# Performance work log

Hardware: AMD Instinct MI355X
Metric: run time of the kernel (lower is better)

The kernel has to match this reference:

```python
import jax, jax.numpy as jnp
import numpy as np

N = 100000      # nodes
E = 1600000     # directed edges (avg degree 16)
F_IN = 256      # dataset.num_node_features
HID = 64        # hidden
C = 40          # dataset.num_classes


def setup_inputs() -> dict:
    key = jax.random.key(0)
    k0, k1, k2, k3 = jax.random.split(key, 4)
    x = jax.random.normal(k0, (N, F_IN), dtype=jnp.float32)
    edge_index = jax.random.randint(k1, (2, E), 0, N, dtype=jnp.int32)
    # Glorot-style init like GCNConv.reset_parameters
    W1 = jax.random.normal(k2, (F_IN, HID), dtype=jnp.float32) * (1.0 / np.sqrt(F_IN))
    b1 = jnp.zeros((HID,), dtype=jnp.float32)
    W2 = jax.random.normal(k3, (HID, C), dtype=jnp.float32) * (1.0 / np.sqrt(HID))
    b2 = jnp.zeros((C,), dtype=jnp.float32)
    return {"x": x, "edge_index": edge_index, "W1": W1, "b1": b1, "W2": W2, "b2": b2}


def gcn_conv(x, row, col, norm, W, b):
    # PyG GCNConv: out[col] += norm * (x @ W)[row]; then + bias
    n = x.shape[0]
    h = x @ W                                   # [N, out]
    msg = h[row] * norm[:, None]                # [E+N, out] gather + scale
    out = jax.ops.segment_sum(msg, col, num_segments=n)  # scatter-add
    return out + b


def _norm_coeffs(edge_index, n, dtype):
    # add self-loops, then symmetric normalization D^{-1/2} A D^{-1/2}
    loop = jnp.arange(n, dtype=edge_index.dtype)
    row = jnp.concatenate([edge_index[0], loop])
    col = jnp.concatenate([edge_index[1], loop])
    deg = jax.ops.segment_sum(jnp.ones_like(col, dtype=dtype), col, num_segments=n)
    dis = jnp.where(deg > 0, jax.lax.rsqrt(jnp.maximum(deg, 1.0)), 0.0)
    return row, col, dis[row] * dis[col]


def reference(x, edge_index, W1, b1, W2, b2):
    n = x.shape[0]
    row, col, norm = _norm_coeffs(edge_index, n, x.dtype)
    h = jax.nn.relu(gcn_conv(x, row, col, norm, W1, b1))
    # F.dropout(p=0.5, training=False) is identity in eval mode
    out = gcn_conv(h, row, col, norm, W2, b2)
    return jax.nn.log_softmax(out, axis=1)
```

## Files before the change

kernel.cpp:

```cpp
#include <hip/hip_runtime.h>
#include <math.h>

#define N_NODES 100000
#define N_EDGES 1600000
#define F_INDIM 256
#define HID 64
#define NCLS 40
#define NBKT 196
#define BKT_CAP 10240
#define EPB 8192
#define ESRC_CAP 1904640

typedef __attribute__((ext_vector_type(8))) short short8;
typedef __attribute__((ext_vector_type(4))) float floatx4;

__device__ __forceinline__ unsigned short f2bf(float f) {
  unsigned u = __float_as_uint(f);
  unsigned r = (u + 0x7FFFu + ((u >> 16) & 1u)) >> 16;
  return (unsigned short)r;
}
__device__ __forceinline__ void add8(float* a, uint4 u) {
  a[0] += __uint_as_float(u.x << 16);
  a[1] += __uint_as_float(u.x & 0xFFFF0000u);
  a[2] += __uint_as_float(u.y << 16);
  a[3] += __uint_as_float(u.y & 0xFFFF0000u);
  a[4] += __uint_as_float(u.z << 16);
  a[5] += __uint_as_float(u.z & 0xFFFF0000u);
  a[6] += __uint_as_float(u.w << 16);
  a[7] += __uint_as_float(u.w & 0xFFFF0000u);
}


__global__ __launch_bounds__(256) void k_zero(int* __restrict__ gcur,
                                              unsigned int* __restrict__ h1bw) {
  int t = threadIdx.x;
  if (t < NBKT) gcur[t] = 0;
  if (t < 32) h1bw[(size_t)N_NODES * 32 + t] = 0;
}


__global__ __launch_bounds__(1024) void k_binA(const int* __restrict__ row,
                                               const int* __restrict__ col,
                                               int* __restrict__ gcur,
                                               unsigned int* __restrict__ bktdata) {
  __shared__ int hist[NBKT];
  __shared__ int cur[NBKT];
  __shared__ int gbase[NBKT];
  const int t = threadIdx.x;
  const int e0 = blockIdx.x * EPB;
  const int n = min(EPB, N_EDGES - e0);
  if (t < NBKT) hist[t] = 0;
  __syncthreads();
  for (int i = t * 4; i < n; i += 4096) {
    int4 c4 = *(const int4*)&col[e0 + i];
    atomicAdd(&hist[c4.x >> 9], 1);
    atomicAdd(&hist[c4.y >> 9], 1);
    atomicAdd(&hist[c4.z >> 9], 1);
    atomicAdd(&hist[c4.w >> 9], 1);
  }
  __syncthreads();
  if (t < NBKT) {
    cur[t] = 0;
    int h = hist[t];
    gbase[t] = (h > 0) ? atomicAdd(&gcur[t], h) : 0;
  }
  __syncthreads();
  for (int i = t * 4; i < n; i += 4096) {
    int4 c4 = *(const int4*)&col[e0 + i];
    int4 r4 = *(const int4*)&row[e0 + i];
#pragma unroll
    for (int k = 0; k < 4; ++k) {
      int c = (k == 0) ? c4.x : (k == 1) ? c4.y : (k == 2) ? c4.z : c4.w;
      int r = (k == 0) ? r4.x : (k == 1) ? r4.y : (k == 2) ? r4.z : r4.w;
      int b = c >> 9;
      int p = atomicAdd(&cur[b], 1);
      bktdata[(size_t)b * BKT_CAP + gbase[b] + p] =
          ((unsigned)(c & 511) << 17) | (unsigned)r;
    }
  }
}


__global__ __launch_bounds__(1024) void k_build2(const int* __restrict__ gcur,
                                                 const unsigned int* __restrict__ bktdata,
                                                 float* __restrict__ dis,
                                                 int* __restrict__ start,
                                                 int* __restrict__ endi,
                                                 int* __restrict__ esrc) {
  __shared__ int h[512];
  __shared__ int cur[512];
  __shared__ int sbase[512];
  __shared__ int wsum[4];
  const int b = blockIdx.x, t = threadIdx.x;
  if (t < 512) { h[t] = 0; cur[t] = 0; }
  if (t < 256) {
    int pv = (t < b) ? (((gcur[t] + 3) & ~3) + 1536) : 0;
#pragma unroll
    for (int off = 1; off < 64; off <<= 1) pv += __shfl_xor(pv, off);
    if ((t & 63) == 0) wsum[t >> 6] = pv;
  }
  __syncthreads();
  const int base = wsum[0] + wsum[1] + wsum[2] + wsum[3];

  const int cnt = gcur[b];
  const unsigned int* p = bktdata + (size_t)b * BKT_CAP;
  for (int i = t; i < cnt; i += 1024) atomicAdd(&h[p[i] >> 17], 1);
  __syncthreads();

  int c0 = 0, p0 = 0;
  if (t < 512) {
    const int n0 = b * 512 + t;
    c0 = h[t];
    p0 = (c0 + 3) & ~3;
    if (n0 < N_NODES) dis[n0] = rsqrtf((float)(c0 + 1));
    h[t] = p0;
  }
  __syncthreads();
#pragma unroll
  for (int off = 1; off < 512; off <<= 1) {
    int u = (t < 512 && t >= off) ? h[t - off] : 0;
    __syncthreads();
    if (t < 512) h[t] += u;
    __syncthreads();
  }
  if (t < 512) {
    const int n0 = b * 512 + t;
    const int sb0 = base + h[t] - p0;
    sbase[t] = sb0;
    if (n0 < N_NODES) { start[n0] = sb0; endi[n0] = sb0 + c0; }
    for (int k = c0; k < p0; ++k) esrc[sb0 + k] = N_NODES;
    if (b == 0 && t == 0) start[N_NODES] = N_EDGES;
  }
  __syncthreads();

  for (int i = t; i < cnt; i += 1024) {
    unsigned u = p[i];
    int ld = u >> 17;
    int src = u & 0x1FFFF;
    int pos = sbase[ld] + atomicAdd(&cur[ld], 1);
    esrc[pos] = src;
  }
}


#define KP 264

__global__ __launch_bounds__(256) void k_gemm1(const float* __restrict__ x,
                                               const float* __restrict__ W1,
                                               const float* __restrict__ dis,
                                               unsigned short* __restrict__ h1b) {
  __shared__ unsigned short wt[HID * KP];
  const int tid = threadIdx.x;
  const int lane = tid & 63;
  const int w = tid >> 6;
  const int quad = lane >> 4;
  const int l15 = lane & 15;
  const int rowBase = blockIdx.x * 64;

#pragma unroll
  for (int i = 0; i < 16; ++i) {
    int f = tid + 256 * i;
    int k = f >> 4;
    int n0 = (f & 15) * 4;
    float4 v = *(const float4*)&W1[(size_t)k * HID + n0];
    wt[(n0 + 0) * KP + k] = f2bf(v.x);
    wt[(n0 + 1) * KP + k] = f2bf(v.y);
    wt[(n0 + 2) * KP + k] = f2bf(v.z);
    wt[(n0 + 3) * KP + k] = f2bf(v.w);
  }
  __syncthreads();

  const int ar = rowBase + w * 16 + l15;
  const float* xrow = x + (size_t)((ar < N_NODES) ? ar : N_NODES - 1) * F_INDIM + quad * 8;

  floatx4 acc[4];
#pragma unroll
  for (int c = 0; c < 4; ++c) acc[c] = (floatx4){0.f, 0.f, 0.f, 0.f};

#pragma unroll
  for (int kc = 0; kc < F_INDIM; kc += 32) {
    const float4 va = *(const float4*)(xrow + kc);
    const float4 vb = *(const float4*)(xrow + kc + 4);
    short8 a;
    a[0] = (short)f2bf(va.x); a[1] = (short)f2bf(va.y);
    a[2] = (short)f2bf(va.z); a[3] = (short)f2bf(va.w);
    a[4] = (short)f2bf(vb.x); a[5] = (short)f2bf(vb.y);
    a[6] = (short)f2bf(vb.z); a[7] = (short)f2bf(vb.w);
#pragma unroll
    for (int c = 0; c < 4; ++c) {
      const short8 b = *(const short8*)&wt[(c * 16 + l15) * KP + kc + quad * 8];
      acc[c] = __builtin_amdgcn_mfma_f32_16x16x32_bf16(a, b, acc[c], 0, 0, 0);
    }
  }

#pragma unroll
  for (int reg = 0; reg < 4; ++reg) {
    int gr = rowBase + w * 16 + quad * 4 + reg;
    if (gr < N_NODES) {
      float d = dis[gr];
#pragma unroll
      for (int c = 0; c < 4; ++c)
        h1b[(size_t)gr * HID + c * 16 + l15] = f2bf(d * acc[c][reg]);
    }
  }
}


__global__ __launch_bounds__(256) void k_agg1(const int* __restrict__ esrc,
                                              const int* __restrict__ start,
                                              const int* __restrict__ endi,
                                              const float* __restrict__ dis,
                                              const unsigned short* __restrict__ h1b,
                                              const float* __restrict__ b1,
                                              unsigned short* __restrict__ ab) {
  int gid = blockIdx.x * 256 + threadIdx.x;
  int node = gid >> 3;
  int q = gid & 7;
  if (node >= N_NODES) return;
  const uint4* hp4 = (const uint4*)h1b;
  const int s = start[node];
  const int epad = (endi[node] + 3) & ~3;
  float acc[8];
#pragma unroll
  for (int j = 0; j < 8; ++j) acc[j] = 0.f;
  int i = s;
  for (; i + 8 <= epad; i += 8) {
    int4 sa = *(const int4*)&esrc[i];
    int4 sb = *(const int4*)&esrc[i + 4];
    uint4 u0 = hp4[(size_t)sa.x * 8 + q];
    uint4 u1 = hp4[(size_t)sa.y * 8 + q];
    uint4 u2 = hp4[(size_t)sa.z * 8 + q];
    uint4 u3 = hp4[(size_t)sa.w * 8 + q];
    uint4 u4 = hp4[(size_t)sb.x * 8 + q];
    uint4 u5 = hp4[(size_t)sb.y * 8 + q];
    uint4 u6 = hp4[(size_t)sb.z * 8 + q];
    uint4 u7 = hp4[(size_t)sb.w * 8 + q];
    add8(acc, u0); add8(acc, u1); add8(acc, u2); add8(acc, u3);
    add8(acc, u4); add8(acc, u5); add8(acc, u6); add8(acc, u7);
  }
  if (i < epad) {
    int4 sv = *(const int4*)&esrc[i];
    uint4 u0 = hp4[(size_t)sv.x * 8 + q];
    uint4 u1 = hp4[(size_t)sv.y * 8 + q];
    uint4 u2 = hp4[(size_t)sv.z * 8 + q];
    uint4 u3 = hp4[(size_t)sv.w * 8 + q];
    add8(acc, u0); add8(acc, u1); add8(acc, u2); add8(acc, u3);
  }
  uint4 us = hp4[(size_t)node * 8 + q];
  add8(acc, us);
  float d = dis[node];
  float4 ba = *(const float4*)&b1[q * 8];
  float4 bb = *(const float4*)&b1[q * 8 + 4];
  float v0 = fmaxf(d * acc[0] + ba.x, 0.f);
  float v1 = fmaxf(d * acc[1] + ba.y, 0.f);
  float v2 = fmaxf(d * acc[2] + ba.z, 0.f);
  float v3 = fmaxf(d * acc[3] + ba.w, 0.f);
  float v4 = fmaxf(d * acc[4] + bb.x, 0.f);
  float v5 = fmaxf(d * acc[5] + bb.y, 0.f);
  float v6 = fmaxf(d * acc[6] + bb.z, 0.f);
  float v7 = fmaxf(d * acc[7] + bb.w, 0.f);
  uint4 o;
  o.x = (unsigned)f2bf(v0) | ((unsigned)f2bf(v1) << 16);
  o.y = (unsigned)f2bf(v2) | ((unsigned)f2bf(v3) << 16);
  o.z = (unsigned)f2bf(v4) | ((unsigned)f2bf(v5) << 16);
  o.w = (unsigned)f2bf(v6) | ((unsigned)f2bf(v7) << 16);
  ((uint4*)ab)[(size_t)node * 8 + q] = o;
}


#define AP 72

__global__ __launch_bounds__(256) void k_gemm2(const unsigned short* __restrict__ ab,
                                               const float* __restrict__ W2,
                                               const float* __restrict__ dis,
                                               unsigned short* __restrict__ gb) {
  __shared__ unsigned short as[64 * AP];
  __shared__ unsigned short w2t[48 * AP];
  const int tid = threadIdx.x;
  const int lane = tid & 63;
  const int w = tid >> 6;
  const int quad = lane >> 4;
  const int l15 = lane & 15;
  const int rowBase = blockIdx.x * 64;

  for (int i = tid; i < 48 * 64; i += 256) {
    int n = i >> 6;
    int k = i & 63;
    w2t[n * AP + k] = (n < NCLS) ? f2bf(W2[(size_t)k * NCLS + n]) : (unsigned short)0;
  }
#pragma unroll
  for (int i = 0; i < 2; ++i) {
    int f = tid + 256 * i;
    int r = f >> 3;
    int q = f & 7;
    int gr = rowBase + r;
    short8 v = (short8){0, 0, 0, 0, 0, 0, 0, 0};
    if (gr < N_NODES) v = *(const short8*)&ab[(size_t)gr * HID + q * 8];
    *(short8*)&as[r * AP + q * 8] = v;
  }
  __syncthreads();

  floatx4 acc[3];
#pragma unroll
  for (int c = 0; c < 3; ++c) acc[c] = (floatx4){0.f, 0.f, 0.f, 0.f};

#pragma unroll
  for (int kh = 0; kh < 2; ++kh) {
    const short8 a = *(const short8*)&as[(w * 16 + l15) * AP + kh * 32 + quad * 8];
#pragma unroll
    for (int c = 0; c < 3; ++c) {
      const short8 b = *(const short8*)&w2t[(c * 16 + l15) * AP + kh * 32 + quad * 8];
      acc[c] = __builtin_amdgcn_mfma_f32_16x16x32_bf16(a, b, acc[c], 0, 0, 0);
    }
  }

#pragma unroll
  for (int reg = 0; reg < 4; ++reg) {
    int gr = rowBase + w * 16 + quad * 4 + reg;
    if (gr < N_NODES) {
      float d = dis[gr];
#pragma unroll
      for (int c = 0; c < 3; ++c) {
        int cc = c * 16 + l15;
        gb[(size_t)gr * 64 + cc] = f2bf(d * acc[c][reg]);
      }
      gb[(size_t)gr * 64 + 48 + l15] = 0;
    }
  }
}


__global__ __launch_bounds__(256) void k_agg2ls(const int* __restrict__ esrc,
                                                const int* __restrict__ start,
                                                const int* __restrict__ endi,
                                                const float* __restrict__ dis,
                                                const unsigned short* __restrict__ gb,
                                                const float* __restrict__ b2,
                                                float* __restrict__ out) {
  int gid = blockIdx.x * 256 + threadIdx.x;
  int node = gid >> 3;
  int q = gid & 7;
  if (node >= N_NODES) return;
  const uint4* gp4 = (const uint4*)gb;
  const int s = start[node];
  const int epad = (endi[node] + 3) & ~3;
  float acc[8];
#pragma unroll
  for (int j = 0; j < 8; ++j) acc[j] = 0.f;
  int i = s;
  for (; i + 8 <= epad; i += 8) {
    int4 sa = *(const int4*)&esrc[i];
    int4 sb = *(const int4*)&esrc[i + 4];
    uint4 u0 = gp4[(size_t)sa.x * 8 + q];
    uint4 u1 = gp4[(size_t)sa.y * 8 + q];
    uint4 u2 = gp4[(size_t)sa.z * 8 + q];
    uint4 u3 = gp4[(size_t)sa.w * 8 + q];
    uint4 u4 = gp4[(size_t)sb.x * 8 + q];
    uint4 u5 = gp4[(size_t)sb.y * 8 + q];
    uint4 u6 = gp4[(size_t)sb.z * 8 + q];
    uint4 u7 = gp4[(size_t)sb.w * 8 + q];
    add8(acc, u0); add8(acc, u1); add8(acc, u2); add8(acc, u3);
    add8(acc, u4); add8(acc, u5); add8(acc, u6); add8(acc, u7);
  }
  if (i < epad) {
    int4 sv = *(const int4*)&esrc[i];
    uint4 u0 = gp4[(size_t)sv.x * 8 + q];
    uint4 u1 = gp4[(size_t)sv.y * 8 + q];
    uint4 u2 = gp4[(size_t)sv.z * 8 + q];
    uint4 u3 = gp4[(size_t)sv.w * 8 + q];
    add8(acc, u0); add8(acc, u1); add8(acc, u2); add8(acc, u3);
  }
  uint4 us = gp4[(size_t)node * 8 + q];
  add8(acc, us);
  const bool wr = q < 5;
  float v0 = 0.f, v1 = 0.f, v2 = 0.f, v3 = 0.f, v4 = 0.f, v5 = 0.f, v6 = 0.f, v7 = 0.f;
  float m = -INFINITY;
  if (wr) {
    float d = dis[node];
    float4 ba = *(const float4*)&b2[q * 8];
    float4 bb = *(const float4*)&b2[q * 8 + 4];
    v0 = d * acc[0] + ba.x;
    v1 = d * acc[1] + ba.y;
    v2 = d * acc[2] + ba.z;
    v3 = d * acc[3] + ba.w;
    v4 = d * acc[4] + bb.x;
    v5 = d * acc[5] + bb.y;
    v6 = d * acc[6] + bb.z;
    v7 = d * acc[7] + bb.w;
    m = fmaxf(fmaxf(fmaxf(v0, v1), fmaxf(v2, v3)),
              fmaxf(fmaxf(v4, v5), fmaxf(v6, v7)));
  }
#pragma unroll
  for (int off = 1; off < 8; off <<= 1) m = fmaxf(m, __shfl_xor(m, off));
  float el = 0.f;
  if (wr) {
    el = __expf(v0 - m) + __expf(v1 - m) + __expf(v2 - m) + __expf(v3 - m) +
         __expf(v4 - m) + __expf(v5 - m) + __expf(v6 - m) + __expf(v7 - m);
  }
#pragma unroll
  for (int off = 1; off < 8; off <<= 1) el += __shfl_xor(el, off);
  float ls = logf(el);
  if (wr) {
    float4 o1 = make_float4(v0 - m - ls, v1 - m - ls, v2 - m - ls, v3 - m - ls);
    float4 o2 = make_float4(v4 - m - ls, v5 - m - ls, v6 - m - ls, v7 - m - ls);
    *(float4*)&out[(size_t)node * NCLS + q * 8] = o1;
    *(float4*)&out[(size_t)node * NCLS + q * 8 + 4] = o2;
  }
}


extern "C" void kernel_launch(void* const* d_in, const int* in_sizes, int n_in,
                              void* d_out, int out_size, void* d_ws, size_t ws_size,
                              hipStream_t stream) {
  const float* x  = (const float*)d_in[0];
  const int*   ei = (const int*)d_in[1];
  const float* W1 = (const float*)d_in[2];
  const float* b1 = (const float*)d_in[3];
  const float* W2 = (const float*)d_in[4];
  const float* b2 = (const float*)d_in[5];
  float* out = (float*)d_out;

  const int* row = ei;
  const int* col = ei + N_EDGES;

  int*            esrc    = (int*)d_ws;
  unsigned int*   bktdata = (unsigned int*)(esrc + ESRC_CAP);
  unsigned short* h1b     = (unsigned short*)(bktdata + (size_t)NBKT * BKT_CAP);
  unsigned short* ab      = h1b + (size_t)(N_NODES + 1) * HID;
  float*          dis     = (float*)(ab + (size_t)N_NODES * HID);
  int*            start   = (int*)(dis + N_NODES);
  int*            endi    = start + N_NODES + 1;
  int*            gcur    = endi + N_NODES;
  unsigned short* gb      = h1b;

  k_zero<<<1, 256, 0, stream>>>(gcur, (unsigned int*)h1b);
  k_binA<<<(N_EDGES + EPB - 1) / EPB, 1024, 0, stream>>>(row, col, gcur, bktdata);
  k_build2<<<NBKT, 1024, 0, stream>>>(gcur, bktdata, dis, start, endi, esrc);

  k_gemm1<<<(N_NODES + 63) / 64, 256, 0, stream>>>(x, W1, dis, h1b);
  k_agg1<<<(N_NODES * 8 + 255) / 256, 256, 0, stream>>>(esrc, start, endi, dis, h1b, b1, ab);

  k_gemm2<<<(N_NODES + 63) / 64, 256, 0, stream>>>(ab, W2, dis, gb);
  k_agg2ls<<<(N_NODES * 8 + 255) / 256, 256, 0, stream>>>(esrc, start, endi, dis, gb, b2, out);
}
```

Baseline: 288.9 us.

## Fuse edge binning with GEMM1 and aggregation1 with GEMM2, drop global atomics

Edge binning and the first GEMM now run as one kernel whose blocks take different roles, so GEMM1 no longer waits on the degree computation. Source-side normalization moves into the aggregation, which reads dis per neighbor. Binning writes fixed-capacity per-block slots instead of using a global atomic cursor, which removes the zeroing kernel. Layer-1 aggregation and GEMM2 are fused through shared memory, cutting launches and the intermediate round trip. The cost is extra per-edge dis loads and fixed capacities (CAPB=96, ECAP) that assume the uniform random degree distribution and can silently drop edges if a per-block bucket overflows.

Result: slower. 316.2 us (+9.5%).

```diff
diff --git a/kernel.cpp b/kernel.cpp
--- a/kernel.cpp
+++ b/kernel.cpp
@@ -7,9 +7,14 @@
 #define HID 64
 #define NCLS 40
 #define NBKT 196
-#define BKT_CAP 10240
+#define NBLKA 196
 #define EPB 8192
-#define ESRC_CAP 1904640
+#define CAPB 96
+#define REGSZ 12544
+#define ECAP 10240
+#define NGEMM1 391
+#define KP 264
+#define AP 72
 
 typedef __attribute__((ext_vector_type(8))) short short8;
 typedef __attribute__((ext_vector_type(4))) float floatx4;
@@ -29,90 +34,158 @@
   a[6] += __uint_as_float(u.w << 16);
   a[7] += __uint_as_float(u.w & 0xFFFF0000u);
 }
-
-
-__global__ __launch_bounds__(256) void k_zero(int* __restrict__ gcur,
-                                              unsigned int* __restrict__ h1bw) {
-  int t = threadIdx.x;
-  if (t < NBKT) gcur[t] = 0;
-  if (t < 32) h1bw[(size_t)N_NODES * 32 + t] = 0;
-}
-
-
-__global__ __launch_bounds__(1024) void k_binA(const int* __restrict__ row,
-                                               const int* __restrict__ col,
-                                               int* __restrict__ gcur,
-                                               unsigned int* __restrict__ bktdata) {
-  __shared__ int hist[NBKT];
-  __shared__ int cur[NBKT];
-  __shared__ int gbase[NBKT];
+__device__ __forceinline__ void fma8(float* a, float d, uint4 u) {
+  a[0] = fmaf(d, __uint_as_float(u.x << 16), a[0]);
+  a[1] = fmaf(d, __uint_as_float(u.x & 0xFFFF0000u), a[1]);
+  a[2] = fmaf(d, __uint_as_float(u.y << 16), a[2]);
+  a[3] = fmaf(d, __uint_as_float(u.y & 0xFFFF0000u), a[3]);
+  a[4] = fmaf(d, __uint_as_float(u.z << 16), a[4]);
+  a[5] = fmaf(d, __uint_as_float(u.z & 0xFFFF0000u), a[5]);
+  a[6] = fmaf(d, __uint_as_float(u.w << 16), a[6]);
+  a[7] = fmaf(d, __uint_as_float(u.w & 0xFFFF0000u), a[7]);
+}
+
+
+__global__ __launch_bounds__(1024) void k_pre(const int* __restrict__ row,
+                                              const int* __restrict__ col,
+                                              const float* __restrict__ x,
+                                              const float* __restrict__ W1,
+                                              unsigned int* __restrict__ bktdata,
+                                              int* __restrict__ cnt,
+                                              unsigned short* __restrict__ h1b) {
+  __shared__ union {
+    int cur[NBKT];
+    unsigned short wt[HID * KP];
+  } sm;
   const int t = threadIdx.x;
-  const int e0 = blockIdx.x * EPB;
-  const int n = min(EPB, N_EDGES - e0);
-  if (t < NBKT) hist[t] = 0;
-  __syncthreads();
-  for (int i = t * 4; i < n; i += 4096) {
-    int4 c4 = *(const int4*)&col[e0 + i];
-    atomicAdd(&hist[c4.x >> 9], 1);
-    atomicAdd(&hist[c4.y >> 9], 1);
-    atomicAdd(&hist[c4.z >> 9], 1);
-    atomicAdd(&hist[c4.w >> 9], 1);
-  }
-  __syncthreads();
-  if (t < NBKT) {
-    cur[t] = 0;
-    int h = hist[t];
-    gbase[t] = (h > 0) ? atomicAdd(&gcur[t], h) : 0;
-  }
-  __syncthreads();
-  for (int i = t * 4; i < n; i += 4096) {
-    int4 c4 = *(const int4*)&col[e0 + i];
-    int4 r4 = *(const int4*)&row[e0 + i];
-#pragma unroll
-    for (int k = 0; k < 4; ++k) {
-      int c = (k == 0) ? c4.x : (k == 1) ? c4.y : (k == 2) ? c4.z : c4.w;
-      int r = (k == 0) ? r4.x : (k == 1) ? r4.y : (k == 2) ? r4.z : r4.w;
-      int b = c >> 9;
-      int p = atomicAdd(&cur[b], 1);
-      bktdata[(size_t)b * BKT_CAP + gbase[b] + p] =
-          ((unsigned)(c & 511) << 17) | (unsigned)r;
-    }
-  }
-}
-
-
-__global__ __launch_bounds__(1024) void k_build2(const int* __restrict__ gcur,
+
+  if (blockIdx.x < NBLKA) {
+    const int blk = blockIdx.x;
+    const int e0 = blk * EPB;
+    const int n = min(EPB, N_EDGES - e0);
+    if (t < NBKT) sm.cur[t] = 0;
+    __syncthreads();
+    for (int i = t * 4; i < n; i += 4096) {
+      int4 c4 = *(const int4*)&col[e0 + i];
+      int4 r4 = *(const int4*)&row[e0 + i];
+#pragma unroll
+      for (int k = 0; k < 4; ++k) {
+        int c = (k == 0) ? c4.x : (k == 1) ? c4.y : (k == 2) ? c4.z : c4.w;
+        int r = (k == 0) ? r4.x : (k == 1) ? r4.y : (k == 2) ? r4.z : r4.w;
+        int b = c >> 9;
+        int p = atomicAdd(&sm.cur[b], 1);
+        if (p < CAPB)
+          bktdata[((size_t)b * NBLKA + blk) * CAPB + p] =
+              ((unsigned)(c & 511) << 17) | (unsigned)r;
+      }
+    }
+    __syncthreads();
+    if (t < NBKT) cnt[t * NBLKA + blk] = min(sm.cur[t], CAPB);
+  } else {
+    const int lane = t & 63;
+    const int w = t >> 6;
+    const int quad = lane >> 4;
+    const int l15 = lane & 15;
+    const int rowBase = (blockIdx.x - NBLKA) * 256;
+#pragma unroll
+    for (int i = 0; i < 4; ++i) {
+      int f = t + 1024 * i;
+      int k = f >> 4;
+      int n0 = (f & 15) * 4;
+      float4 v = *(const float4*)&W1[(size_t)k * HID + n0];
+      sm.wt[(n0 + 0) * KP + k] = f2bf(v.x);
+      sm.wt[(n0 + 1) * KP + k] = f2bf(v.y);
+      sm.wt[(n0 + 2) * KP + k] = f2bf(v.z);
+      sm.wt[(n0 + 3) * KP + k] = f2bf(v.w);
+    }
+    __syncthreads();
+
+    const int ar = rowBase + w * 16 + l15;
+    const float* xrow =
+        x + (size_t)((ar < N_NODES) ? ar : N_NODES - 1) * F_INDIM + quad * 8;
+
+    floatx4 acc[4];
+#pragma unroll
+    for (int c = 0; c < 4; ++c) acc[c] = (floatx4){0.f, 0.f, 0.f, 0.f};
+
+#pragma unroll
+    for (int kc = 0; kc < F_INDIM; kc += 32) {
+      const float4 va = *(const float4*)(xrow + kc);
+      const float4 vb = *(const float4*)(xrow + kc + 4);
+      short8 a;
+      a[0] = (short)f2bf(va.x); a[1] = (short)f2bf(va.y);
+      a[2] = (short)f2bf(va.z); a[3] = (short)f2bf(va.w);
+      a[4] = (short)f2bf(vb.x); a[5] = (short)f2bf(vb.y);
+      a[6] = (short)f2bf(vb.z); a[7] = (short)f2bf(vb.w);
+#pragma unroll
+      for (int c = 0; c < 4; ++c) {
+        const short8 bfr = *(const short8*)&sm.wt[(c * 16 + l15) * KP + kc + quad * 8];
+        acc[c] = __builtin_amdgcn_mfma_f32_16x16x32_bf16(a, bfr, acc[c], 0, 0, 0);
+      }
+    }
+
+#pragma unroll
+    for (int reg = 0; reg < 4; ++reg) {
+      int gr = rowBase + w * 16 + quad * 4 + reg;
+      if (gr <= N_NODES) {
+        bool real = gr < N_NODES;
+#pragma unroll
+        for (int c = 0; c < 4; ++c)
+          h1b[(size_t)gr * HID + c * 16 + l15] =
+              real ? f2bf(acc[c][reg]) : (unsigned short)0;
+      }
+    }
+  }
+}
+
+
+__global__ __launch_bounds__(1024) void k_build2(const int* __restrict__ cnt,
                                                  const unsigned int* __restrict__ bktdata,
                                                  float* __restrict__ dis,
                                                  int* __restrict__ start,
                                                  int* __restrict__ endi,
                                                  int* __restrict__ esrc) {
+  __shared__ int scnt[NBLKA];
+  __shared__ int sscan[NBLKA];
+  __shared__ unsigned int ecache[ECAP];
   __shared__ int h[512];
-  __shared__ int cur[512];
+  __shared__ int curs[512];
   __shared__ int sbase[512];
-  __shared__ int wsum[4];
   const int b = blockIdx.x, t = threadIdx.x;
-  if (t < 512) { h[t] = 0; cur[t] = 0; }
-  if (t < 256) {
-    int pv = (t < b) ? (((gcur[t] + 3) & ~3) + 1536) : 0;
-#pragma unroll
-    for (int off = 1; off < 64; off <<= 1) pv += __shfl_xor(pv, off);
-    if ((t & 63) == 0) wsum[t >> 6] = pv;
-  }
-  __syncthreads();
-  const int base = wsum[0] + wsum[1] + wsum[2] + wsum[3];
-
-  const int cnt = gcur[b];
-  const unsigned int* p = bktdata + (size_t)b * BKT_CAP;
-  for (int i = t; i < cnt; i += 1024) atomicAdd(&h[p[i] >> 17], 1);
+
+  if (t < 512) { h[t] = 0; curs[t] = 0; }
+  if (t < NBLKA) { int c = cnt[b * NBLKA + t]; scnt[t] = c; sscan[t] = c; }
+  __syncthreads();
+#pragma unroll
+  for (int off = 1; off < NBLKA; off <<= 1) {
+    int u = (t < NBLKA && t >= off) ? sscan[t - off] : 0;
+    __syncthreads();
+    if (t < NBLKA) sscan[t] += u;
+    __syncthreads();
+  }
+  const int total = min(sscan[NBLKA - 1], ECAP);
+
+  for (int j = t; j < total; j += 1024) {
+    int lo = 0, hi = NBLKA - 1;
+    while (lo < hi) {
+      int mid = (lo + hi) >> 1;
+      if (sscan[mid] <= j) lo = mid + 1; else hi = mid;
+    }
+    int segoff = j - (sscan[lo] - scnt[lo]);
+    ecache[j] = bktdata[((size_t)b * NBLKA + lo) * CAPB + segoff];
+  }
+  __syncthreads();
+
+  for (int i = t; i < total; i += 1024) atomicAdd(&h[ecache[i] >> 17], 1);
   __syncthreads();
 
   int c0 = 0, p0 = 0;
   if (t < 512) {
     const int n0 = b * 512 + t;
     c0 = h[t];
-    p0 = (c0 + 3) & ~3;
+    p0 = (c0 + 7) & ~7;
     if (n0 < N_NODES) dis[n0] = rsqrtf((float)(c0 + 1));
+    else if (n0 == N_NODES) dis[n0] = 0.f;
     h[t] = p0;
   }
   __syncthreads();
@@ -125,206 +198,116 @@
   }
   if (t < 512) {
     const int n0 = b * 512 + t;
-    const int sb0 = base + h[t] - p0;
+    const int sb0 = b * REGSZ + h[t] - p0;
     sbase[t] = sb0;
     if (n0 < N_NODES) { start[n0] = sb0; endi[n0] = sb0 + c0; }
     for (int k = c0; k < p0; ++k) esrc[sb0 + k] = N_NODES;
-    if (b == 0 && t == 0) start[N_NODES] = N_EDGES;
-  }
-  __syncthreads();
-
-  for (int i = t; i < cnt; i += 1024) {
-    unsigned u = p[i];
+  }
+  __syncthreads();
+
+  for (int i = t; i < total; i += 1024) {
+    unsigned u = ecache[i];
     int ld = u >> 17;
     int src = u & 0x1FFFF;
-    int pos = sbase[ld] + atomicAdd(&cur[ld], 1);
+    int pos = sbase[ld] + atomicAdd(&curs[ld], 1);
     esrc[pos] = src;
   }
 }
 
 
-#define KP 264
-
-__global__ __launch_bounds__(256) void k_gemm1(const float* __restrict__ x,
-                                               const float* __restrict__ W1,
-                                               const float* __restrict__ dis,
-                                               unsigned short* __restrict__ h1b) {
-  __shared__ unsigned short wt[HID * KP];
-  const int tid = threadIdx.x;
-  const int lane = tid & 63;
-  const int w = tid >> 6;
-  const int quad = lane >> 4;
-  const int l15 = lane & 15;
-  const int rowBase = blockIdx.x * 64;
-
-#pragma unroll
-  for (int i = 0; i < 16; ++i) {
-    int f = tid + 256 * i;
-    int k = f >> 4;
-    int n0 = (f & 15) * 4;
-    float4 v = *(const float4*)&W1[(size_t)k * HID + n0];
-    wt[(n0 + 0) * KP + k] = f2bf(v.x);
-    wt[(n0 + 1) * KP + k] = f2bf(v.y);
-    wt[(n0 + 2) * KP + k] = f2bf(v.z);
-    wt[(n0 + 3) * KP + k] = f2bf(v.w);
-  }
-  __syncthreads();
-
-  const int ar = rowBase + w * 16 + l15;
-  const float* xrow = x + (size_t)((ar < N_NODES) ? ar : N_NODES - 1) * F_INDIM + quad * 8;
-
-  floatx4 acc[4];
-#pragma unroll
-  for (int c = 0; c < 4; ++c) acc[c] = (floatx4){0.f, 0.f, 0.f, 0.f};
-
-#pragma unroll
-  for (int kc = 0; kc < F_INDIM; kc += 32) {
-    const float4 va = *(const float4*)(xrow + kc);
-    const float4 vb = *(const float4*)(xrow + kc + 4);
-    short8 a;
-    a[0] = (short)f2bf(va.x); a[1] = (short)f2bf(va.y);
-    a[2] = (short)f2bf(va.z); a[3] = (short)f2bf(va.w);
-    a[4] = (short)f2bf(vb.x); a[5] = (short)f2bf(vb.y);
-    a[6] = (short)f2bf(vb.z); a[7] = (short)f2bf(vb.w);
-#pragma unroll
-    for (int c = 0; c < 4; ++c) {
-      const short8 b = *(const short8*)&wt[(c * 16 + l15) * KP + kc + quad * 8];
-      acc[c] = __builtin_amdgcn_mfma_f32_16x16x32_bf16(a, b, acc[c], 0, 0, 0);
-    }
-  }
-
-#pragma unroll
-  for (int reg = 0; reg < 4; ++reg) {
-    int gr = rowBase + w * 16 + quad * 4 + reg;
-    if (gr < N_NODES) {
-      float d = dis[gr];
-#pragma unroll
-      for (int c = 0; c < 4; ++c)
-        h1b[(size_t)gr * HID + c * 16 + l15] = f2bf(d * acc[c][reg]);
-    }
-  }
-}
-
-
-__global__ __launch_bounds__(256) void k_agg1(const int* __restrict__ esrc,
-                                              const int* __restrict__ start,
-                                              const int* __restrict__ endi,
-                                              const float* __restrict__ dis,
-                                              const unsigned short* __restrict__ h1b,
-                                              const float* __restrict__ b1,
-                                              unsigned short* __restrict__ ab) {
-  int gid = blockIdx.x * 256 + threadIdx.x;
-  int node = gid >> 3;
-  int q = gid & 7;
-  if (node >= N_NODES) return;
-  const uint4* hp4 = (const uint4*)h1b;
-  const int s = start[node];
-  const int epad = (endi[node] + 3) & ~3;
-  float acc[8];
-#pragma unroll
-  for (int j = 0; j < 8; ++j) acc[j] = 0.f;
-  int i = s;
-  for (; i + 8 <= epad; i += 8) {
-    int4 sa = *(const int4*)&esrc[i];
-    int4 sb = *(const int4*)&esrc[i + 4];
-    uint4 u0 = hp4[(size_t)sa.x * 8 + q];
-    uint4 u1 = hp4[(size_t)sa.y * 8 + q];
-    uint4 u2 = hp4[(size_t)sa.z * 8 + q];
-    uint4 u3 = hp4[(size_t)sa.w * 8 + q];
-    uint4 u4 = hp4[(size_t)sb.x * 8 + q];
-    uint4 u5 = hp4[(size_t)sb.y * 8 + q];
-    uint4 u6 = hp4[(size_t)sb.z * 8 + q];
-    uint4 u7 = hp4[(size_t)sb.w * 8 + q];
-    add8(acc, u0); add8(acc, u1); add8(acc, u2); add8(acc, u3);
-    add8(acc, u4); add8(acc, u5); add8(acc, u6); add8(acc, u7);
-  }
-  if (i < epad) {
-    int4 sv = *(const int4*)&esrc[i];
-    uint4 u0 = hp4[(size_t)sv.x * 8 + q];
-    uint4 u1 = hp4[(size_t)sv.y * 8 + q];
-    uint4 u2 = hp4[(size_t)sv.z * 8 + q];
-    uint4 u3 = hp4[(size_t)sv.w * 8 + q];
-    add8(acc, u0); add8(acc, u1); add8(acc, u2); add8(acc, u3);
-  }
-  uint4 us = hp4[(size_t)node * 8 + q];
-  add8(acc, us);
-  float d = dis[node];
-  float4 ba = *(const float4*)&b1[q * 8];
-  float4 bb = *(const float4*)&b1[q * 8 + 4];
-  float v0 = fmaxf(d * acc[0] + ba.x, 0.f);
-  float v1 = fmaxf(d * acc[1] + ba.y, 0.f);
-  float v2 = fmaxf(d * acc[2] + ba.z, 0.f);
-  float v3 = fmaxf(d * acc[3] + ba.w, 0.f);
-  float v4 = fmaxf(d * acc[4] + bb.x, 0.f);
-  float v5 = fmaxf(d * acc[5] + bb.y, 0.f);
-  float v6 = fmaxf(d * acc[6] + bb.z, 0.f);
-  float v7 = fmaxf(d * acc[7] + bb.w, 0.f);
-  uint4 o;
-  o.x = (unsigned)f2bf(v0) | ((unsigned)f2bf(v1) << 16);
-  o.y = (unsigned)f2bf(v2) | ((unsigned)f2bf(v3) << 16);
-  o.z = (unsigned)f2bf(v4) | ((unsigned)f2bf(v5) << 16);
-  o.w = (unsigned)f2bf(v6) | ((unsigned)f2bf(v7) << 16);
-  ((uint4*)ab)[(size_t)node * 8 + q] = o;
-}
-
-
-#define AP 72
-
-__global__ __launch_bounds__(256) void k_gemm2(const unsigned short* __restrict__ ab,
-                                               const float* __restrict__ W2,
-                                               const float* __restrict__ dis,
-                                               unsigned short* __restrict__ gb) {
+__global__ __launch_bounds__(512) void k_agg1g2(const int* __restrict__ esrc,
+                                                const int* __restrict__ start,
+                                                const int* __restrict__ endi,
+                                                const float* __restrict__ dis,
+                                                const unsigned short* __restrict__ h1b,
+                                                const float* __restrict__ b1,
+                                                const float* __restrict__ W2,
+                                                unsigned short* __restrict__ gb) {
   __shared__ unsigned short as[64 * AP];
   __shared__ unsigned short w2t[48 * AP];
-  const int tid = threadIdx.x;
-  const int lane = tid & 63;
-  const int w = tid >> 6;
-  const int quad = lane >> 4;
-  const int l15 = lane & 15;
-  const int rowBase = blockIdx.x * 64;
-
-  for (int i = tid; i < 48 * 64; i += 256) {
-    int n = i >> 6;
+  const int t = threadIdx.x;
+  const int nodeBase = blockIdx.x * 64;
+  const int node = nodeBase + (t >> 3);
+  const int q = t & 7;
+
+  for (int i = t; i < 48 * 64; i += 512) {
+    int nn = i >> 6;
     int k = i & 63;
-    w2t[n * AP + k] = (n < NCLS) ? f2bf(W2[(size_t)k * NCLS + n]) : (unsigned short)0;
-  }
-#pragma unroll
-  for (int i = 0; i < 2; ++i) {
-    int f = tid + 256 * i;
-    int r = f >> 3;
-    int q = f & 7;
-    int gr = rowBase + r;
-    short8 v = (short8){0, 0, 0, 0, 0, 0, 0, 0};
-    if (gr < N_NODES) v = *(const short8*)&ab[(size_t)gr * HID + q * 8];
-    *(short8*)&as[r * AP + q * 8] = v;
-  }
-  __syncthreads();
-
-  floatx4 acc[3];
-#pragma unroll
-  for (int c = 0; c < 3; ++c) acc[c] = (floatx4){0.f, 0.f, 0.f, 0.f};
-
-#pragma unroll
-  for (int kh = 0; kh < 2; ++kh) {
-    const short8 a = *(const short8*)&as[(w * 16 + l15) * AP + kh * 32 + quad * 8];
-#pragma unroll
-    for (int c = 0; c < 3; ++c) {
-      const short8 b = *(const short8*)&w2t[(c * 16 + l15) * AP + kh * 32 + quad * 8];
-      acc[c] = __builtin_amdgcn_mfma_f32_16x16x32_bf16(a, b, acc[c], 0, 0, 0);
-    }
-  }
-
-#pragma unroll
-  for (int reg = 0; reg < 4; ++reg) {
-    int gr = rowBase + w * 16 + quad * 4 + reg;
-    if (gr < N_NODES) {
-      float d = dis[gr];
+    w2t[nn * AP + k] = (nn < NCLS) ? f2bf(W2[(size_t)k * NCLS + nn]) : (unsigned short)0;
+  }
+
+  uint4 o = (uint4){0u, 0u, 0u, 0u};
+  if (node < N_NODES) {
+    const uint4* hp4 = (const uint4*)h1b;
+    const int s = start[node];
+    const int e8 = (endi[node] + 7) & ~7;
+    float acc[8];
+#pragma unroll
+    for (int j = 0; j < 8; ++j) acc[j] = 0.f;
+    for (int i = s; i < e8; i += 8) {
+      int4 sa = *(const int4*)&esrc[i];
+      int4 sb = *(const int4*)&esrc[i + 4];
+      float d0 = dis[sa.x], d1 = dis[sa.y], d2 = dis[sa.z], d3 = dis[sa.w];
+      float d4 = dis[sb.x], d5 = dis[sb.y], d6 = dis[sb.z], d7 = dis[sb.w];
+      uint4 u0 = hp4[(size_t)sa.x * 8 + q];
+      uint4 u1 = hp4[(size_t)sa.y * 8 + q];
+      uint4 u2 = hp4[(size_t)sa.z * 8 + q];
+      uint4 u3 = hp4[(size_t)sa.w * 8 + q];
+      uint4 u4 = hp4[(size_t)sb.x * 8 + q];
+      uint4 u5 = hp4[(size_t)sb.y * 8 + q];
+      uint4 u6 = hp4[(size_t)sb.z * 8 + q];
+      uint4 u7 = hp4[(size_t)sb.w * 8 + q];
+      fma8(acc, d0, u0); fma8(acc, d1, u1); fma8(acc, d2, u2); fma8(acc, d3, u3);
+      fma8(acc, d4, u4); fma8(acc, d5, u5); fma8(acc, d6, u6); fma8(acc, d7, u7);
+    }
+    const float dn = dis[node];
+    uint4 us = hp4[(size_t)node * 8 + q];
+    fma8(acc, dn, us);
+    float4 ba = *(const float4*)&b1[q * 8];
+    float4 bb = *(const float4*)&b1[q * 8 + 4];
+    float v0 = fmaxf(dn * acc[0] + ba.x, 0.f);
+    float v1 = fmaxf(dn * acc[1] + ba.y, 0.f);
+    float v2 = fmaxf(dn * acc[2] + ba.z, 0.f);
+    float v3 = fmaxf(dn * acc[3] + ba.w, 0.f);
+    float v4 = fmaxf(dn * acc[4] + bb.x, 0.f);
+    float v5 = fmaxf(dn * acc[5] + bb.y, 0.f);
+    float v6 = fmaxf(dn * acc[6] + bb.z, 0.f);
+    float v7 = fmaxf(dn * acc[7] + bb.w, 0.f);
+    o.x = (unsigned)f2bf(v0) | ((unsigned)f2bf(v1) << 16);
+    o.y = (unsigned)f2bf(v2) | ((unsigned)f2bf(v3) << 16);
+    o.z = (unsigned)f2bf(v4) | ((unsigned)f2bf(v5) << 16);
+    o.w = (unsigned)f2bf(v6) | ((unsigned)f2bf(v7) << 16);
+  }
+  *(uint4*)&as[(t >> 3) * AP + q * 8] = o;
+  __syncthreads();
+
+  const int lane = t & 63;
+  const int w = t >> 6;
+  if (w < 4) {
+    const int quad = lane >> 4;
+    const int l15 = lane & 15;
+    floatx4 acc2[3];
+#pragma unroll
+    for (int c = 0; c < 3; ++c) acc2[c] = (floatx4){0.f, 0.f, 0.f, 0.f};
+#pragma unroll
+    for (int kh = 0; kh < 2; ++kh) {
+      const short8 a = *(const short8*)&as[(w * 16 + l15) * AP + kh * 32 + quad * 8];
 #pragma unroll
       for (int c = 0; c < 3; ++c) {
-        int cc = c * 16 + l15;
-        gb[(size_t)gr * 64 + cc] = f2bf(d * acc[c][reg]);
+        const short8 bfr = *(const short8*)&w2t[(c * 16 + l15) * AP + kh * 32 + quad * 8];
+        acc2[c] = __builtin_amdgcn_mfma_f32_16x16x32_bf16(a, bfr, acc2[c], 0, 0, 0);
       }
-      gb[(size_t)gr * 64 + 48 + l15] = 0;
+    }
+#pragma unroll
+    for (int reg = 0; reg < 4; ++reg) {
+      int gr = nodeBase + w * 16 + quad * 4 + reg;
+      if (gr <= N_NODES) {
+        float dd = dis[gr];
+#pragma unroll
+        for (int c = 0; c < 3; ++c)
+          gb[(size_t)gr * 64 + c * 16 + l15] = f2bf(dd * acc2[c][reg]);
+        gb[(size_t)gr * 64 + 48 + l15] = 0;
+      }
     }
   }
 }
@@ -343,12 +326,11 @@
   if (node >= N_NODES) return;
   const uint4* gp4 = (const uint4*)gb;
   const int s = start[node];
-  const int epad = (endi[node] + 3) & ~3;
+  const int e8 = (endi[node] + 7) & ~7;
   float acc[8];
 #pragma unroll
   for (int j = 0; j < 8; ++j) acc[j] = 0.f;
-  int i = s;
-  for (; i + 8 <= epad; i += 8) {
+  for (int i = s; i < e8; i += 8) {
     int4 sa = *(const int4*)&esrc[i];
     int4 sb = *(const int4*)&esrc[i + 4];
     uint4 u0 = gp4[(size_t)sa.x * 8 + q];
@@ -361,14 +343,6 @@
     uint4 u7 = gp4[(size_t)sb.w * 8 + q];
     add8(acc, u0); add8(acc, u1); add8(acc, u2); add8(acc, u3);
     add8(acc, u4); add8(acc, u5); add8(acc, u6); add8(acc, u7);
-  }
-  if (i < epad) {
-    int4 sv = *(const int4*)&esrc[i];
-    uint4 u0 = gp4[(size_t)sv.x * 8 + q];
-    uint4 u1 = gp4[(size_t)sv.y * 8 + q];
-    uint4 u2 = gp4[(size_t)sv.z * 8 + q];
-    uint4 u3 = gp4[(size_t)sv.w * 8 + q];
-    add8(acc, u0); add8(acc, u1); add8(acc, u2); add8(acc, u3);
   }
   uint4 us = gp4[(size_t)node * 8 + q];
   add8(acc, us);
@@ -424,22 +398,16 @@
   const int* col = ei + N_EDGES;
 
   int*            esrc    = (int*)d_ws;
-  unsigned int*   bktdata = (unsigned int*)(esrc + ESRC_CAP);
-  unsigned short* h1b     = (unsigned short*)(bktdata + (size_t)NBKT * BKT_CAP);
-  unsigned short* ab      = h1b + (size_t)(N_NODES + 1) * HID;
-  float*          dis     = (float*)(ab + (size_t)N_NODES * HID);
-  int*            start   = (int*)(dis + N_NODES);
+  unsigned int*   bktdata = (unsigned int*)(esrc + (size_t)NBKT * REGSZ);
+  int*            cnt     = (int*)(bktdata + (size_t)NBKT * NBLKA * CAPB);
+  unsigned short* h1b     = (unsigned short*)(cnt + NBKT * NBLKA);
+  unsigned short* gb      = h1b + (size_t)(N_NODES + 1) * HID;
+  float*          dis     = (float*)(gb + (size_t)(N_NODES + 1) * HID);
+  int*            start   = (int*)(dis + N_NODES + 1);
   int*            endi    = start + N_NODES + 1;
-  int*            gcur    = endi + N_NODES;
-  unsigned short* gb      = h1b;
-
-  k_zero<<<1, 256, 0, stream>>>(gcur, (unsigned int*)h1b);
-  k_binA<<<(N_EDGES + EPB - 1) / EPB, 1024, 0, stream>>>(row, col, gcur, bktdata);
-  k_build2<<<NBKT, 1024, 0, stream>>>(gcur, bktdata, dis, start, endi, esrc);
-
-  k_gemm1<<<(N_NODES + 63) / 64, 256, 0, stream>>>(x, W1, dis, h1b);
-  k_agg1<<<(N_NODES * 8 + 255) / 256, 256, 0, stream>>>(esrc, start, endi, dis, h1b, b1, ab);
-
-  k_gemm2<<<(N_NODES + 63) / 64, 256, 0, stream>>>(ab, W2, dis, gb);
+
+  k_pre<<<NBLKA + NGEMM1, 1024, 0, stream>>>(row, col, x, W1, bktdata, cnt, h1b);
+  k_build2<<<NBKT, 1024, 0, stream>>>(cnt, bktdata, dis, start, endi, esrc);
+  k_agg1g2<<<(N_NODES + 63) / 64, 512, 0, stream>>>(esrc, start, endi, dis, h1b, b1, W2, gb);
   k_agg2ls<<<(N_NODES * 8 + 255) / 256, 256, 0, stream>>>(esrc, start, endi, dis, gb, b2, out);
 }
```
